# Optimization experiments

Hardware: AMD Instinct MI355X
Metric: run time of the kernel (lower is better)

## Reference

```python
import jax, jax.numpy as jnp
import numpy as np

H = 12        # num heads
DH = 64       # head dim
W = 8         # window size
WIN2 = W * W  # tokens per window


def _relative_position_index():
    # Swin-style relative position index, [WIN2, WIN2] int array (static).
    coords = np.stack(np.meshgrid(np.arange(W), np.arange(W), indexing='ij'))  # [2,W,W]
    flat = coords.reshape(2, -1)                                               # [2,WIN2]
    rel = flat[:, :, None] - flat[:, None, :]                                  # [2,WIN2,WIN2]
    rel = rel.transpose(1, 2, 0).astype(np.int64)
    rel[..., 0] += W - 1
    rel[..., 1] += W - 1
    rel[..., 0] *= 2 * W - 1
    return rel.sum(-1)  # [WIN2, WIN2]


def setup_inputs() -> dict:
    key = jax.random.key(0)
    ks = jax.random.split(key, 12)
    B, S, D = 128, 256, 768
    scale = 0.02
    return {
        'q': jax.random.normal(ks[0], (B, S, D), jnp.float32),
        'k': jax.random.normal(ks[1], (B, S, D), jnp.float32),
        'v': jax.random.normal(ks[2], (B, S, D), jnp.float32),
        'Wq': jax.random.normal(ks[3], (D, D), jnp.float32) * scale,
        'bq': jnp.zeros((D,), jnp.float32),
        'Wk': jax.random.normal(ks[4], (D, D), jnp.float32) * scale,
        'bk': jnp.zeros((D,), jnp.float32),
        'Wv': jax.random.normal(ks[5], (D, D), jnp.float32) * scale,
        'bv': jnp.zeros((D,), jnp.float32),
        'Wo': jax.random.normal(ks[6], (D, D), jnp.float32) * scale,
        'bo': jnp.zeros((D,), jnp.float32),
        'bias_table': jax.random.normal(ks[7], ((2 * W - 1) ** 2, H), jnp.float32) * scale,
    }


def reference(q, k, v, Wq, bq, Wk, bk, Wv, bv, Wo, bo, bias_table):
    B, S, D = q.shape

    def proj(x, Wt, bt):
        # Linear stores weight as [out, in]; y = x @ W^T + b, then split heads.
        return (x @ Wt.T + bt).reshape(B, S, H, DH).transpose(0, 2, 1, 3)

    qh = proj(q, Wq, bq)  # [B,H,S,DH]
    kh = proj(k, Wk, bk)
    vh = proj(v, Wv, bv)

    scores = jnp.einsum('bhqd,bhkd->bhqk', qh, kh) / np.float32(np.sqrt(DH))

    idx = _relative_position_index()                         # static [WIN2,WIN2]
    bias = bias_table[idx.reshape(-1)].reshape(WIN2, WIN2, H)
    bias = bias.transpose(2, 0, 1)                           # [H,WIN2,WIN2]
    n_contrast = S // WIN2
    bias = jnp.tile(bias, (1, n_contrast, n_contrast))       # [H,S,S]

    probs = jax.nn.softmax(scores + bias[None], axis=-1)     # dropout p=0 (eval)
    ctx = jnp.einsum('bhqk,bhkd->bhqd', probs, vh)
    ctx = ctx.transpose(0, 2, 1, 3).reshape(B, S, D)
    return ctx @ Wo.T + bo
```

## Files before the change

kernel.cpp:

```cpp
#include <hip/hip_runtime.h>


typedef __bf16 bf16;
typedef __bf16 bf16x8 __attribute__((ext_vector_type(8)));
typedef float  f32x4  __attribute__((ext_vector_type(4)));

#define MFMA_BF16(a, b, c) __builtin_amdgcn_mfma_f32_16x16x32_bf16((a), (b), (c), 0, 0, 0)

__device__ __forceinline__ void gld16(const void* g, void* l) {
    __builtin_amdgcn_global_load_lds(
        (const __attribute__((address_space(1))) void*)g,
        (__attribute__((address_space(3))) void*)l, 16, 0, 0);
}

__device__ __forceinline__ bf16x8 pack8(f32x4 lo, f32x4 hi) {
    bf16x8 r;
    r[0] = (bf16)lo[0]; r[1] = (bf16)lo[1]; r[2] = (bf16)lo[2]; r[3] = (bf16)lo[3];
    r[4] = (bf16)hi[0]; r[5] = (bf16)hi[1]; r[6] = (bf16)hi[2]; r[7] = (bf16)hi[3];
    return r;
}

__device__ __forceinline__ int swz8(int row, int g) { return g ^ (row & 7); }

__global__ __launch_bounds__(256)
void cvt_f32_bf16(const float* __restrict__ src, bf16* __restrict__ dst, int ngroups)
{
    int i = blockIdx.x * 256 + threadIdx.x;
    const int stride = gridDim.x * 256;
    for (; i < ngroups; i += stride) {
        const f32x4* s = (const f32x4*)(src + (size_t)i * 8);
        *(bf16x8*)(dst + (size_t)i * 8) = pack8(s[0], s[1]);
    }
}

__global__ __launch_bounds__(256)
void gemm_qkv_b(const bf16* __restrict__ X, const bf16* __restrict__ Wb,
                const float* __restrict__ bias, bf16* __restrict__ out)
{
    __shared__ bf16 As[2][128 * 64];
    __shared__ bf16 Bs[2][128 * 64];

    const int wg  = blockIdx.x;
    const int pos = wg >> 3;
    const int mi  = (wg & 7) * 32 + pos / 6;
    const int ni  = pos % 6;
    const int m0  = mi * 128;
    const int n0  = ni * 128;

    const int tid  = threadIdx.x;
    const int w    = tid >> 6;
    const int lane = tid & 63;
    const int quad = lane >> 4;
    const int l15  = lane & 15;
    const int wr   = (w >> 1) * 64;
    const int wc   = (w & 1) * 64;

    f32x4 acc[4][4] = {};

    auto stage = [&](int buf, int k0) {
        #pragma unroll
        for (int p = 0; p < 4; ++p) {
            int g = p * 256 + tid;
            int row = g >> 3, slot = g & 7;
            int cg  = slot ^ (row & 7);
            gld16(X  + (size_t)(m0 + row) * 768 + k0 + cg * 8, (char*)&As[buf][0] + g * 16);
            gld16(Wb + (size_t)(n0 + row) * 768 + k0 + cg * 8, (char*)&Bs[buf][0] + g * 16);
        }
    };
    auto compute = [&](int buf) {
        #pragma unroll
        for (int kk = 0; kk < 2; ++kk) {
            bf16x8 af[4], bfr[4];
            #pragma unroll
            for (int mt = 0; mt < 4; ++mt) {
                int row = wr + mt * 16 + l15;
                af[mt] = *(const bf16x8*)&As[buf][row * 64 + swz8(row, kk * 4 + quad) * 8];
            }
            #pragma unroll
            for (int nt = 0; nt < 4; ++nt) {
                int row = wc + nt * 16 + l15;
                bfr[nt] = *(const bf16x8*)&Bs[buf][row * 64 + swz8(row, kk * 4 + quad) * 8];
            }
            #pragma unroll
            for (int mt = 0; mt < 4; ++mt)
                #pragma unroll
                for (int nt = 0; nt < 4; ++nt)
                    acc[mt][nt] = MFMA_BF16(af[mt], bfr[nt], acc[mt][nt]);
        }
    };

    stage(0, 0);
    __syncthreads();
    int cur = 0;
    for (int kt = 0; kt < 11; ++kt) {
        stage(cur ^ 1, (kt + 1) * 64);
        compute(cur);
        __syncthreads();
        cur ^= 1;
    }
    compute(cur);

    #pragma unroll
    for (int mt = 0; mt < 4; ++mt) {
        #pragma unroll
        for (int nt = 0; nt < 4; ++nt) {
            int gn = n0 + wc + nt * 16 + l15;
            float bv = bias[gn];
            int h = gn >> 6, d = gn & 63;
            #pragma unroll
            for (int r = 0; r < 4; ++r) {
                int gm = m0 + wr + mt * 16 + quad * 4 + r;
                int b = gm >> 8, s = gm & 255;
                out[(((size_t)(b * 12 + h) << 8) + s) * 64 + d] = (bf16)(acc[mt][nt][r] + bv);
            }
        }
    }
}

__global__ __launch_bounds__(256)
void gemm_out_b(const bf16* __restrict__ X, const bf16* __restrict__ Wb,
                const float* __restrict__ bias, float* __restrict__ out)
{
    __shared__ bf16 As[2][128 * 64];
    __shared__ bf16 Bs[2][128 * 64];

    const int wg  = blockIdx.x;
    const int pos = wg >> 3;
    const int mi  = (wg & 7) * 32 + pos / 6;
    const int ni  = pos % 6;
    const int m0  = mi * 128;
    const int n0  = ni * 128;

    const int tid  = threadIdx.x;
    const int w    = tid >> 6;
    const int lane = tid & 63;
    const int quad = lane >> 4;
    const int l15  = lane & 15;
    const int wr   = (w >> 1) * 64;
    const int wc   = (w & 1) * 64;

    f32x4 acc[4][4] = {};

    auto stage = [&](int buf, int k0) {
        #pragma unroll
        for (int p = 0; p < 4; ++p) {
            int g = p * 256 + tid;
            int row = g >> 3, slot = g & 7;
            int cg  = slot ^ (row & 7);
            gld16(X  + (size_t)(m0 + row) * 768 + k0 + cg * 8, (char*)&As[buf][0] + g * 16);
            gld16(Wb + (size_t)(n0 + row) * 768 + k0 + cg * 8, (char*)&Bs[buf][0] + g * 16);
        }
    };
    auto compute = [&](int buf) {
        #pragma unroll
        for (int kk = 0; kk < 2; ++kk) {
            bf16x8 af[4], bfr[4];
            #pragma unroll
            for (int mt = 0; mt < 4; ++mt) {
                int row = wr + mt * 16 + l15;
                af[mt] = *(const bf16x8*)&As[buf][row * 64 + swz8(row, kk * 4 + quad) * 8];
            }
            #pragma unroll
            for (int nt = 0; nt < 4; ++nt) {
                int row = wc + nt * 16 + l15;
                bfr[nt] = *(const bf16x8*)&Bs[buf][row * 64 + swz8(row, kk * 4 + quad) * 8];
            }
            #pragma unroll
            for (int mt = 0; mt < 4; ++mt)
                #pragma unroll
                for (int nt = 0; nt < 4; ++nt)
                    acc[mt][nt] = MFMA_BF16(af[mt], bfr[nt], acc[mt][nt]);
        }
    };

    stage(0, 0);
    __syncthreads();
    int cur = 0;
    for (int kt = 0; kt < 11; ++kt) {
        stage(cur ^ 1, (kt + 1) * 64);
        compute(cur);
        __syncthreads();
        cur ^= 1;
    }
    compute(cur);

    #pragma unroll
    for (int mt = 0; mt < 4; ++mt) {
        #pragma unroll
        for (int nt = 0; nt < 4; ++nt) {
            int gn = n0 + wc + nt * 16 + l15;
            float bv = bias[gn];
            #pragma unroll
            for (int r = 0; r < 4; ++r) {
                int gm = m0 + wr + mt * 16 + quad * 4 + r;
                out[(size_t)gm * 768 + gn] = acc[mt][nt][r] + bv;
            }
        }
    }
}

__global__ __launch_bounds__(256)
void transpose_v(const bf16* __restrict__ vh, bf16* __restrict__ vt)
{
    __shared__ bf16 Ts[64 * 65];
    const int qt = blockIdx.x, h = blockIdx.y, b = blockIdx.z;
    const bf16* src = vh + ((size_t)(b * 12 + h) * 256 + qt * 64) * 64;
    bf16* dst = vt + (size_t)(b * 12 + h) * 64 * 256;

    const int tid = threadIdx.x;
    {
        int row = tid >> 2, c0 = (tid & 3) * 16;
        bf16x8 v0 = *(const bf16x8*)(src + row * 64 + c0);
        bf16x8 v1 = *(const bf16x8*)(src + row * 64 + c0 + 8);
        #pragma unroll
        for (int i = 0; i < 8; ++i) {
            Ts[row * 65 + c0 + i]     = v0[i];
            Ts[row * 65 + c0 + 8 + i] = v1[i];
        }
    }
    __syncthreads();
    {
        int d = tid >> 2, j0 = (tid & 3) * 16;
        bf16x8 o0, o1;
        #pragma unroll
        for (int i = 0; i < 8; ++i) {
            o0[i] = Ts[(j0 + i) * 65 + d];
            o1[i] = Ts[(j0 + 8 + i) * 65 + d];
        }
        *(bf16x8*)(dst + (size_t)d * 256 + qt * 64 + j0)     = o0;
        *(bf16x8*)(dst + (size_t)d * 256 + qt * 64 + j0 + 8) = o1;
    }
}

__global__ __launch_bounds__(256)
void attn_kernel(const bf16* __restrict__ qh, const bf16* __restrict__ kh,
                 const bf16* __restrict__ vt, const float* __restrict__ table,
                 bf16* __restrict__ ctx)
{
    __shared__ bf16 Qs[64 * 64];
    __shared__ bf16 Ks[64 * 64];
    __shared__ bf16 Vs[64 * 64];
    __shared__ bf16 Ps[4 * 16 * 72];
    __shared__ bf16 Bsh[64 * 68];

    const int tid  = threadIdx.x;
    const int qt   = blockIdx.x;
    const int h    = blockIdx.y;
    const int b    = blockIdx.z;
    const int w    = tid >> 6;
    const int lane = tid & 63;
    const int quad = lane >> 4;
    const int l15  = lane & 15;

    const size_t bh = (size_t)(b * 12 + h) * 256 * 64;
    const bf16* Qg  = qh + bh + (size_t)qt * 64 * 64;
    const bf16* Kg  = kh + bh;
    const bf16* Vtg = vt + bh;

    #pragma unroll
    for (int p = 0; p < 2; ++p) {
        int g = p * 256 + tid;
        gld16(Qg + (size_t)(g >> 3) * 64 + (g & 7) * 8, (char*)Qs + g * 16);
    }
    {
        int i = tid >> 2, j0 = (tid & 3) * 16;
        int ai = i >> 3, aj = i & 7;
        #pragma unroll
        for (int jj = 0; jj < 16; ++jj) {
            int j = j0 + jj;
            int idx = (ai - (j >> 3) + 7) * 15 + (aj - (j & 7) + 7);
            Bsh[i * 68 + j] = (bf16)table[idx * 12 + h];
        }
    }

    f32x4 sacc[16] = {};
    bf16x8 qf0, qf1;
    for (int c = 0; c < 4; ++c) {
        __syncthreads();
        #pragma unroll
        for (int p = 0; p < 2; ++p) {
            int g = p * 256 + tid;
            gld16(Kg + (size_t)(c * 64 + (g >> 3)) * 64 + (g & 7) * 8, (char*)Ks + g * 16);
        }
        __syncthreads();
        if (c == 0) {
            qf0 = *(const bf16x8*)&Qs[(w * 16 + l15) * 64 + quad * 8];
            qf1 = *(const bf16x8*)&Qs[(w * 16 + l15) * 64 + 32 + quad * 8];
        }
        #pragma unroll
        for (int jtl = 0; jtl < 4; ++jtl) {
            bf16x8 kf0 = *(const bf16x8*)&Ks[(jtl * 16 + l15) * 64 + quad * 8];
            bf16x8 kf1 = *(const bf16x8*)&Ks[(jtl * 16 + l15) * 64 + 32 + quad * 8];
            sacc[c * 4 + jtl] = MFMA_BF16(qf0, kf0, sacc[c * 4 + jtl]);
            sacc[c * 4 + jtl] = MFMA_BF16(qf1, kf1, sacc[c * 4 + jtl]);
        }
    }

    const int browbase = w * 16 + quad * 4;
    float p[16][4];
    #pragma unroll
    for (int jt = 0; jt < 16; ++jt) {
        int jcol = ((jt * 16) & 63) + l15;
        #pragma unroll
        for (int r = 0; r < 4; ++r)
            p[jt][r] = sacc[jt][r] * 0.125f + (float)Bsh[(browbase + r) * 68 + jcol];
    }
    float invl[4];
    #pragma unroll
    for (int r = 0; r < 4; ++r) {
        float m = p[0][r];
        #pragma unroll
        for (int jt = 1; jt < 16; ++jt) m = fmaxf(m, p[jt][r]);
        #pragma unroll
        for (int off = 1; off < 16; off <<= 1)
            m = fmaxf(m, __shfl_xor(m, off, 64));
        float s = 0.f;
        #pragma unroll
        for (int jt = 0; jt < 16; ++jt) {
            p[jt][r] = __expf(p[jt][r] - m);
            s += p[jt][r];
        }
        #pragma unroll
        for (int off = 1; off < 16; off <<= 1)
            s += __shfl_xor(s, off, 64);
        invl[r] = 1.0f / s;
    }

    f32x4 cacc[4] = {};
    bf16* Pw = &Ps[w * 16 * 72];
    for (int c = 0; c < 4; ++c) {
        __syncthreads();
        #pragma unroll
        for (int pp = 0; pp < 2; ++pp) {
            int g = pp * 256 + tid;
            gld16(Vtg + (size_t)(g >> 3) * 256 + c * 64 + (g & 7) * 8, (char*)Vs + g * 16);
        }
        #pragma unroll
        for (int jtl = 0; jtl < 4; ++jtl) {
            int jt = c * 4 + jtl;
            #pragma unroll
            for (int r = 0; r < 4; ++r)
                Pw[(quad * 4 + r) * 72 + jtl * 16 + l15] = (bf16)(p[jt][r] * invl[r]);
        }
        __syncthreads();
        bf16x8 pf0 = *(const bf16x8*)&Pw[l15 * 72 + quad * 8];
        bf16x8 pf1 = *(const bf16x8*)&Pw[l15 * 72 + 32 + quad * 8];
        #pragma unroll
        for (int dt = 0; dt < 4; ++dt) {
            bf16x8 vf0 = *(const bf16x8*)&Vs[(dt * 16 + l15) * 64 + quad * 8];
            bf16x8 vf1 = *(const bf16x8*)&Vs[(dt * 16 + l15) * 64 + 32 + quad * 8];
            cacc[dt] = MFMA_BF16(pf0, vf0, cacc[dt]);
            cacc[dt] = MFMA_BF16(pf1, vf1, cacc[dt]);
        }
    }

    const size_t obase = ((size_t)b * 256) * 768 + (size_t)h * 64;
    #pragma unroll
    for (int dt = 0; dt < 4; ++dt) {
        #pragma unroll
        for (int r = 0; r < 4; ++r) {
            int s = qt * 64 + w * 16 + quad * 4 + r;
            int d = dt * 16 + l15;
            ctx[obase + (size_t)s * 768 + d] = (bf16)cacc[dt][r];
        }
    }
}

extern "C" void kernel_launch(void* const* d_in, const int* in_sizes, int n_in,
                              void* d_out, int out_size, void* d_ws, size_t ws_size,
                              hipStream_t stream) {
    (void)in_sizes; (void)n_in; (void)out_size; (void)ws_size;
    const float* q     = (const float*)d_in[0];
    const float* k     = (const float*)d_in[1];
    const float* v     = (const float*)d_in[2];
    const float* Wq    = (const float*)d_in[3];
    const float* bq    = (const float*)d_in[4];
    const float* Wk    = (const float*)d_in[5];
    const float* bk    = (const float*)d_in[6];
    const float* Wv    = (const float*)d_in[7];
    const float* bv    = (const float*)d_in[8];
    const float* Wo    = (const float*)d_in[9];
    const float* bo    = (const float*)d_in[10];
    const float* table = (const float*)d_in[11];

    const size_t NE = (size_t)128 * 256 * 768;
    const size_t WE = (size_t)768 * 768;

    bf16* qh  = (bf16*)d_ws;
    bf16* kh  = qh + NE;
    bf16* vh  = kh + NE;
    bf16* vt  = vh + NE;
    bf16* ctx = vh;
    float* out = (float*)d_out;

    bf16* xq_b = (bf16*)d_out;
    bf16* xk_b = xq_b + NE;
    bf16* xv_b = xq_b;
    bf16* wq_b = vt;
    bf16* wk_b = wq_b + WE;
    bf16* wv_b = wk_b + WE;
    bf16* wo_b = qh;

    const int XG = (int)(NE / 8);
    const int WG = (int)(WE / 8);

    dim3 blk(256);
    cvt_f32_bf16<<<2048, blk, 0, stream>>>(q,  xq_b, XG);
    cvt_f32_bf16<<<2048, blk, 0, stream>>>(k,  xk_b, XG);
    cvt_f32_bf16<<<288,  blk, 0, stream>>>(Wq, wq_b, WG);
    cvt_f32_bf16<<<288,  blk, 0, stream>>>(Wk, wk_b, WG);
    cvt_f32_bf16<<<288,  blk, 0, stream>>>(Wv, wv_b, WG);

    gemm_qkv_b<<<1536, blk, 0, stream>>>(xq_b, wq_b, bq, qh);
    gemm_qkv_b<<<1536, blk, 0, stream>>>(xk_b, wk_b, bk, kh);
    cvt_f32_bf16<<<2048, blk, 0, stream>>>(v, xv_b, XG);
    gemm_qkv_b<<<1536, blk, 0, stream>>>(xv_b, wv_b, bv, vh);

    transpose_v<<<dim3(4, 12, 128), blk, 0, stream>>>(vh, vt);
    attn_kernel<<<dim3(4, 12, 128), blk, 0, stream>>>(qh, kh, vt, table, ctx);

    cvt_f32_bf16<<<288, blk, 0, stream>>>(Wo, wo_b, WG);
    gemm_out_b<<<1536, blk, 0, stream>>>(ctx, wo_b, bo, out);
}
```

Baseline: 709.0 us.

## Double-buffer K/V loads, swizzle LDS, and precompute relative-position bias per head

Moves relative-position bias expansion into a separate small kernel that writes a bf16 [H,64,64] table once, so the attention kernel reads 16 bias values per thread into registers instead of rebuilding an LDS tile from gathered table reads in every block. K and V tiles are double-buffered in a shared LDS pair, with the next chunk's async load issued before the current chunk's MFMAs. An XOR swizzle is applied to the Q/K/V LDS layouts to reduce bank conflicts. It adds one tiny kernel launch and reuses part of the output buffer as scratch for the bias.

```diff
diff --git a/kernel.cpp b/kernel.cpp
--- a/kernel.cpp
+++ b/kernel.cpp
@@ -30,6 +30,23 @@
     for (; i < ngroups; i += stride) {
         const f32x4* s = (const f32x4*)(src + (size_t)i * 8);
         *(bf16x8*)(dst + (size_t)i * 8) = pack8(s[0], s[1]);
+    }
+}
+
+__global__ __launch_bounds__(256)
+void bias_expand(const float* __restrict__ table, bf16* __restrict__ biasb)
+{
+    const int h   = blockIdx.x;
+    const int tid = threadIdx.x;
+    const int e0  = tid * 16;
+    const int i   = e0 >> 6;
+    const int j0  = e0 & 63;
+    const int ai  = i >> 3, aj = i & 7;
+    #pragma unroll
+    for (int n = 0; n < 16; ++n) {
+        int j = j0 + n;
+        int idx = (ai - (j >> 3) + 7) * 15 + (aj - (j & 7) + 7);
+        biasb[h * 4096 + i * 64 + j] = (bf16)table[idx * 12 + h];
     }
 }
 
@@ -234,14 +251,12 @@
 
 __global__ __launch_bounds__(256)
 void attn_kernel(const bf16* __restrict__ qh, const bf16* __restrict__ kh,
-                 const bf16* __restrict__ vt, const float* __restrict__ table,
+                 const bf16* __restrict__ vt, const bf16* __restrict__ biasb,
                  bf16* __restrict__ ctx)
 {
     __shared__ bf16 Qs[64 * 64];
-    __shared__ bf16 Ks[64 * 64];
-    __shared__ bf16 Vs[64 * 64];
+    __shared__ bf16 KVs[2][64 * 64];
     __shared__ bf16 Ps[4 * 16 * 72];
-    __shared__ bf16 Bsh[64 * 68];
 
     const int tid  = threadIdx.x;
     const int qt   = blockIdx.x;
@@ -257,54 +272,59 @@
     const bf16* Kg  = kh + bh;
     const bf16* Vtg = vt + bh;
 
-    #pragma unroll
-    for (int p = 0; p < 2; ++p) {
-        int g = p * 256 + tid;
-        gld16(Qg + (size_t)(g >> 3) * 64 + (g & 7) * 8, (char*)Qs + g * 16);
-    }
-    {
-        int i = tid >> 2, j0 = (tid & 3) * 16;
-        int ai = i >> 3, aj = i & 7;
-        #pragma unroll
-        for (int jj = 0; jj < 16; ++jj) {
-            int j = j0 + jj;
-            int idx = (ai - (j >> 3) + 7) * 15 + (aj - (j & 7) + 7);
-            Bsh[i * 68 + j] = (bf16)table[idx * 12 + h];
-        }
-    }
-
-    f32x4 sacc[16] = {};
-    bf16x8 qf0, qf1;
-    for (int c = 0; c < 4; ++c) {
-        __syncthreads();
+    auto stageT = [&](const bf16* src, size_t rs, bf16* dstLds) {
         #pragma unroll
         for (int p = 0; p < 2; ++p) {
             int g = p * 256 + tid;
-            gld16(Kg + (size_t)(c * 64 + (g >> 3)) * 64 + (g & 7) * 8, (char*)Ks + g * 16);
-        }
-        __syncthreads();
-        if (c == 0) {
-            qf0 = *(const bf16x8*)&Qs[(w * 16 + l15) * 64 + quad * 8];
-            qf1 = *(const bf16x8*)&Qs[(w * 16 + l15) * 64 + 32 + quad * 8];
-        }
+            int row = g >> 3, slot = g & 7;
+            int cg  = slot ^ (row & 7);
+            gld16(src + (size_t)row * rs + cg * 8, (char*)dstLds + g * 16);
+        }
+    };
+
+    const int browbase = w * 16 + quad * 4;
+    const bf16* bb = biasb + h * 4096;
+    float bregs[4][4];
+    #pragma unroll
+    for (int r = 0; r < 4; ++r)
+        #pragma unroll
+        for (int c4 = 0; c4 < 4; ++c4)
+            bregs[r][c4] = (float)bb[(browbase + r) * 64 + c4 * 16 + l15];
+
+    stageT(Qg, 64, Qs);
+    stageT(Kg, 64, KVs[0]);
+    __syncthreads();
+
+    bf16x8 qf0, qf1;
+    {
+        int qrow = w * 16 + l15;
+        qf0 = *(const bf16x8*)&Qs[qrow * 64 + swz8(qrow, quad) * 8];
+        qf1 = *(const bf16x8*)&Qs[qrow * 64 + swz8(qrow, 4 + quad) * 8];
+    }
+
+    f32x4 sacc[16] = {};
+    for (int c = 0; c < 4; ++c) {
+        if (c < 3) stageT(Kg + (size_t)(c + 1) * 64 * 64, 64, KVs[(c + 1) & 1]);
+        const bf16* Kb = KVs[c & 1];
         #pragma unroll
         for (int jtl = 0; jtl < 4; ++jtl) {
-            bf16x8 kf0 = *(const bf16x8*)&Ks[(jtl * 16 + l15) * 64 + quad * 8];
-            bf16x8 kf1 = *(const bf16x8*)&Ks[(jtl * 16 + l15) * 64 + 32 + quad * 8];
+            int krow = jtl * 16 + l15;
+            bf16x8 kf0 = *(const bf16x8*)&Kb[krow * 64 + swz8(krow, quad) * 8];
+            bf16x8 kf1 = *(const bf16x8*)&Kb[krow * 64 + swz8(krow, 4 + quad) * 8];
             sacc[c * 4 + jtl] = MFMA_BF16(qf0, kf0, sacc[c * 4 + jtl]);
             sacc[c * 4 + jtl] = MFMA_BF16(qf1, kf1, sacc[c * 4 + jtl]);
         }
-    }
-
-    const int browbase = w * 16 + quad * 4;
+        __syncthreads();
+    }
+
+    stageT(Vtg, 256, KVs[0]);
+
     float p[16][4];
     #pragma unroll
-    for (int jt = 0; jt < 16; ++jt) {
-        int jcol = ((jt * 16) & 63) + l15;
+    for (int jt = 0; jt < 16; ++jt)
         #pragma unroll
         for (int r = 0; r < 4; ++r)
-            p[jt][r] = sacc[jt][r] * 0.125f + (float)Bsh[(browbase + r) * 68 + jcol];
-    }
+            p[jt][r] = sacc[jt][r] * 0.125f + bregs[r][jt & 3];
     float invl[4];
     #pragma unroll
     for (int r = 0; r < 4; ++r) {
@@ -329,12 +349,6 @@
     f32x4 cacc[4] = {};
     bf16* Pw = &Ps[w * 16 * 72];
     for (int c = 0; c < 4; ++c) {
-        __syncthreads();
-        #pragma unroll
-        for (int pp = 0; pp < 2; ++pp) {
-            int g = pp * 256 + tid;
-            gld16(Vtg + (size_t)(g >> 3) * 256 + c * 64 + (g & 7) * 8, (char*)Vs + g * 16);
-        }
         #pragma unroll
         for (int jtl = 0; jtl < 4; ++jtl) {
             int jt = c * 4 + jtl;
@@ -343,12 +357,15 @@
                 Pw[(quad * 4 + r) * 72 + jtl * 16 + l15] = (bf16)(p[jt][r] * invl[r]);
         }
         __syncthreads();
+        if (c < 3) stageT(Vtg + (size_t)(c + 1) * 64, 256, KVs[(c + 1) & 1]);
+        const bf16* Vb = KVs[c & 1];
         bf16x8 pf0 = *(const bf16x8*)&Pw[l15 * 72 + quad * 8];
         bf16x8 pf1 = *(const bf16x8*)&Pw[l15 * 72 + 32 + quad * 8];
         #pragma unroll
         for (int dt = 0; dt < 4; ++dt) {
-            bf16x8 vf0 = *(const bf16x8*)&Vs[(dt * 16 + l15) * 64 + quad * 8];
-            bf16x8 vf1 = *(const bf16x8*)&Vs[(dt * 16 + l15) * 64 + 32 + quad * 8];
+            int vrow = dt * 16 + l15;
+            bf16x8 vf0 = *(const bf16x8*)&Vb[vrow * 64 + swz8(vrow, quad) * 8];
+            bf16x8 vf1 = *(const bf16x8*)&Vb[vrow * 64 + swz8(vrow, 4 + quad) * 8];
             cacc[dt] = MFMA_BF16(pf0, vf0, cacc[dt]);
             cacc[dt] = MFMA_BF16(pf1, vf1, cacc[dt]);
         }
@@ -393,13 +410,14 @@
     bf16* ctx = vh;
     float* out = (float*)d_out;
 
-    bf16* xq_b = (bf16*)d_out;
-    bf16* xk_b = xq_b + NE;
-    bf16* xv_b = xq_b;
-    bf16* wq_b = vt;
-    bf16* wk_b = wq_b + WE;
-    bf16* wv_b = wk_b + WE;
-    bf16* wo_b = qh;
+    bf16* xq_b  = (bf16*)d_out;
+    bf16* xk_b  = xq_b + NE;
+    bf16* xv_b  = xq_b;
+    bf16* biasb = xk_b;
+    bf16* wq_b  = vt;
+    bf16* wk_b  = wq_b + WE;
+    bf16* wv_b  = wk_b + WE;
+    bf16* wo_b  = qh;
 
     const int XG = (int)(NE / 8);
     const int WG = (int)(WE / 8);
@@ -413,11 +431,12 @@
 
     gemm_qkv_b<<<1536, blk, 0, stream>>>(xq_b, wq_b, bq, qh);
     gemm_qkv_b<<<1536, blk, 0, stream>>>(xk_b, wk_b, bk, kh);
+    bias_expand<<<12, blk, 0, stream>>>(table, biasb);
     cvt_f32_bf16<<<2048, blk, 0, stream>>>(v, xv_b, XG);
     gemm_qkv_b<<<1536, blk, 0, stream>>>(xv_b, wv_b, bv, vh);
 
     transpose_v<<<dim3(4, 12, 128), blk, 0, stream>>>(vh, vt);
-    attn_kernel<<<dim3(4, 12, 128), blk, 0, stream>>>(qh, kh, vt, table, ctx);
+    attn_kernel<<<dim3(4, 12, 128), blk, 0, stream>>>(qh, kh, vt, biasb, ctx);
 
     cvt_f32_bf16<<<288, blk, 0, stream>>>(Wo, wo_b, WG);
     gemm_out_b<<<1536, blk, 0, stream>>>(ctx, wo_b, bo, out);
```

Result: faster. 685.5 us (-3.3%).
